# Optimization experiments

Hardware: AMD Instinct MI355X
Metric: run time of the kernel (lower is better)

## Reference

```python
import jax, jax.numpy as jnp
import numpy as np

D_MODEL = 1024
N_HEADS = 16
D_K = D_MODEL // N_HEADS


def setup_inputs() -> dict:
    key = jax.random.key(0)
    ks = jax.random.split(key, 9)
    s = 1.0 / np.sqrt(D_MODEL)
    x = jax.random.normal(ks[0], (2, 2048, D_MODEL), dtype=jnp.float32)
    Wq = jax.random.uniform(ks[1], (D_MODEL, D_MODEL), jnp.float32, -s, s)
    bq = jax.random.uniform(ks[2], (D_MODEL,), jnp.float32, -s, s)
    Wk = jax.random.uniform(ks[3], (D_MODEL, D_MODEL), jnp.float32, -s, s)
    bk = jax.random.uniform(ks[4], (D_MODEL,), jnp.float32, -s, s)
    Wv = jax.random.uniform(ks[5], (D_MODEL, D_MODEL), jnp.float32, -s, s)
    bv = jax.random.uniform(ks[6], (D_MODEL,), jnp.float32, -s, s)
    Wo = jax.random.uniform(ks[7], (D_MODEL, D_MODEL), jnp.float32, -s, s)
    bo = jax.random.uniform(ks[8], (D_MODEL,), jnp.float32, -s, s)
    return {"x": x, "Wq": Wq, "bq": bq, "Wk": Wk, "bk": bk,
            "Wv": Wv, "bv": bv, "Wo": Wo, "bo": bo}


def reference(x, Wq, bq, Wk, bk, Wv, bv, Wo, bo):
    B, S, _ = x.shape
    # torch Linear: y = x @ W.T + b
    def proj(W, b):
        h = x @ W.T + b                       # [B,S,D]
        return h.reshape(B, S, N_HEADS, D_K).transpose(0, 2, 1, 3)  # [B,H,S,dk]
    Q, K, V = proj(Wq, bq), proj(Wk, bk), proj(Wv, bv)
    scale = 1.0 / np.sqrt(D_K).astype(np.float32)
    scores = jnp.einsum('bhqd,bhkd->bhqk', Q, K) * scale  # [B,H,S,S]
    causal = jnp.tril(jnp.ones((S, S), dtype=bool))
    scores = jnp.where(causal, scores, -jnp.inf)
    attn = jax.nn.softmax(scores, axis=-1)
    ctx = jnp.einsum('bhqk,bhkd->bhqd', attn, V)          # [B,H,S,dk]
    ctx = ctx.transpose(0, 2, 1, 3).reshape(B, S, D_MODEL)
    return ctx @ Wo.T + bo
```

## Files before the change

### kernel.cpp

```cpp
#include <hip/hip_runtime.h>
#include <stdint.h>

#define D_MODEL 1024
#define NHEADS  16
#define DKH     64
#define BATCH   2
#define SEQ     2048
#define NTOK    (BATCH*SEQ)

typedef unsigned short u16;
typedef __attribute__((ext_vector_type(8))) short short8;
typedef __attribute__((ext_vector_type(4))) float f32x4;
typedef __attribute__((ext_vector_type(16))) float f32x16;
typedef __attribute__((ext_vector_type(2))) unsigned int u32x2;
typedef __attribute__((address_space(1))) unsigned int as1_u32;
typedef __attribute__((address_space(3))) unsigned int as3_u32;

__device__ __forceinline__ u16 f2bf(float f) {
  unsigned int i = __float_as_uint(f);
  i += 0x7FFF + ((i >> 16) & 1);
  return (u16)(i >> 16);
}
__device__ __forceinline__ f32x4 mfma_bf16(short8 a, short8 b, f32x4 c) {
  return __builtin_amdgcn_mfma_f32_16x16x32_bf16(a, b, c, 0, 0, 0);
}
__device__ __forceinline__ f32x16 mfma32(short8 a, short8 b, f32x16 c) {
  return __builtin_amdgcn_mfma_f32_32x32x16_bf16(a, b, c, 0, 0, 0);
}
__device__ __forceinline__ void gload_lds16(const u16* g, u16* l) {
  __builtin_amdgcn_global_load_lds((as1_u32*)g, (as3_u32*)l, 16, 0, 0);
}
__device__ __forceinline__ short8 ld_frag(const u16* p) {
  short8 v; __builtin_memcpy(&v, __builtin_assume_aligned(p, 16), 16); return v;
}
__device__ __forceinline__ uint32_t pk_bf16_trunc(float hi, float lo) {
  return __builtin_amdgcn_perm(__float_as_uint(hi), __float_as_uint(lo), 0x07060302u);
}

#define QSCALE 0.18033688011112042f
#define M0LOG2 4.32808512266689f

__global__ __launch_bounds__(256)
void convert_kernel(const float* __restrict__ x,  const float* __restrict__ wq,
                    const float* __restrict__ wk, const float* __restrict__ wv,
                    const float* __restrict__ wo,
                    u16* __restrict__ xb,  u16* __restrict__ wqb,
                    u16* __restrict__ wkb, u16* __restrict__ wvb,
                    u16* __restrict__ wob)
{
  const int q = blockIdx.x * 256 + threadIdx.x;
  const float* src; u16* dst; int local;
  if (q < 1048576) { src = x; dst = xb; local = q; }
  else {
    const int t = q - 1048576, r = t >> 18;
    local = t & 262143;
    src = (r == 0) ? wq : (r == 1) ? wk : (r == 2) ? wv : wo;
    dst = (r == 0) ? wqb : (r == 1) ? wkb : (r == 2) ? wvb : wob;
  }
  float f[4];
  __builtin_memcpy(f, src + (size_t)local * 4, 16);
  uint32_t o[2];
  o[0] = ((uint32_t)f2bf(f[1]) << 16) | f2bf(f[0]);
  o[1] = ((uint32_t)f2bf(f[3]) << 16) | f2bf(f[2]);
  __builtin_memcpy(dst + (size_t)local * 4, o, 8);
}

__device__ __forceinline__ void gemm_core_bf16(
    const u16* __restrict__ A, const u16* __restrict__ Bt,
    int m0, int n0, u16* As, u16* Bs, f32x4 (&acc)[4][4])
{
  const int tid  = threadIdx.x;
  const int wave = tid >> 6, lane = tid & 63;
  const int quad = lane >> 4, l15 = lane & 15;
  const int wm = wave & 1, wn = wave >> 1;
  const int srow = lane >> 2;
  const int scol = (lane & 3) << 3;

#pragma unroll
  for (int i = 0; i < 4; i++)
#pragma unroll
    for (int j = 0; j < 4; j++) acc[i][j] = (f32x4){0.f, 0.f, 0.f, 0.f};

  for (int k0 = 0; k0 < D_MODEL; k0 += 32) {
    __syncthreads();
#pragma unroll
    for (int is = 0; is < 2; is++) {
      const int rbase = (is * 4 + wave) * 16;
      gload_lds16(A  + (size_t)(m0 + rbase + srow) * D_MODEL + k0 + scol, As + rbase * 32);
      gload_lds16(Bt + (size_t)(n0 + rbase + srow) * D_MODEL + k0 + scol, Bs + rbase * 32);
    }
    __syncthreads();

    short8 aF[4], bF[4];
#pragma unroll
    for (int i = 0; i < 4; i++)
      aF[i] = ld_frag(As + (wm * 64 + i * 16 + l15) * 32 + quad * 8);
#pragma unroll
    for (int j = 0; j < 4; j++)
      bF[j] = ld_frag(Bs + (wn * 64 + j * 16 + l15) * 32 + quad * 8);
#pragma unroll
    for (int i = 0; i < 4; i++)
#pragma unroll
      for (int j = 0; j < 4; j++)
        acc[i][j] = mfma_bf16(aF[i], bF[j], acc[i][j]);
  }
}

__global__ __launch_bounds__(256)
void qkv_proj_kernel(const u16* __restrict__ xb,
                     const u16* __restrict__ Wqb, const u16* __restrict__ Wkb,
                     const u16* __restrict__ Wvb,
                     const float* __restrict__ bq, const float* __restrict__ bk,
                     const float* __restrict__ bv,
                     u16* __restrict__ qplane, u16* __restrict__ kplane,
                     u16* __restrict__ vplane)
{
  __shared__ __align__(16) u16 SMEM[16384];
  u16* As = SMEM;
  u16* Bs = SMEM + 4096;

  const int m0  = blockIdx.x * 128;
  const int by  = blockIdx.y;
  const int mat = by >> 3;
  const int n0  = (by & 7) * 128;
  const u16* W      = (mat == 0) ? Wqb : (mat == 1) ? Wkb : Wvb;
  const float* bias = (mat == 0) ? bq : (mat == 1) ? bk : bv;

  f32x4 acc[4][4];
  gemm_core_bf16(xb, W, m0, n0, As, Bs, acc);

  const int tid = threadIdx.x, wave = tid >> 6, lane = tid & 63;
  const int quad = lane >> 4, l15 = lane & 15;
  const int wm = wave & 1, wn = wave >> 1;

  if (mat == 0) {
#pragma unroll
    for (int j = 0; j < 4; j++) {
      const int gcol = n0 + wn * 64 + j * 16 + l15;
      const float bias_v = bias[gcol];
      const int h = gcol >> 6, dj = gcol & 63;
#pragma unroll
      for (int i = 0; i < 4; i++) {
#pragma unroll
        for (int r = 0; r < 4; r++) {
          const int grow = m0 + wm * 64 + i * 16 + quad * 4 + r;
          const int b = grow >> 11, s = grow & (SEQ - 1);
          const float v = (acc[i][j][r] + bias_v) * QSCALE;
          qplane[(((size_t)(b * NHEADS + h)) * SEQ + s) * DKH + dj] = f2bf(v);
        }
      }
    }
    return;
  }

  u16* Stg = SMEM;
  __syncthreads();
  const int t4 = (wn * 2 + wm) * 4096;

  if (mat == 1) {
#pragma unroll
    for (int j = 0; j < 4; j++) {
      const int dj = j * 16 + l15;
      const float bias_v = bias[n0 + wn * 64 + dj];
#pragma unroll
      for (int i = 0; i < 4; i++) {
#pragma unroll
        for (int r = 0; r < 4; r++) {
          const int rr = i * 16 + quad * 4 + r;
          Stg[t4 + rr * 64 + (dj ^ ((rr & 7) << 3))] = f2bf(acc[i][j][r] + bias_v);
        }
      }
    }
  } else {
#pragma unroll
    for (int j = 0; j < 4; j++) {
      const int dj = j * 16 + l15;
      const float bias_v = bias[n0 + wn * 64 + dj];
      const int vswz = (dj & 7) << 3;
#pragma unroll
      for (int i = 0; i < 4; i++) {
        const int kkb = i * 16 + quad * 4;
        uint32_t w[2];
        w[0] = ((uint32_t)f2bf(acc[i][j][1] + bias_v) << 16) | f2bf(acc[i][j][0] + bias_v);
        w[1] = ((uint32_t)f2bf(acc[i][j][3] + bias_v) << 16) | f2bf(acc[i][j][2] + bias_v);
        __builtin_memcpy(__builtin_assume_aligned(
            Stg + t4 + dj * 64 + (kkb ^ vswz), 8), w, 8);
      }
    }
  }
  __syncthreads();

  const int tloc = tid >> 6, cl = tid & 63;
  const int hh = tloc >> 1, tt = tloc & 1;
  const int b  = m0 >> 11;
  const int h  = (n0 >> 6) + hh;
  const int kt = ((m0 & (SEQ - 1)) >> 6) + tt;
  u16* gdst = ((mat == 1) ? kplane : vplane)
              + (((size_t)(b * NHEADS + h)) * 32 + kt) * 4096;
  const u16* lsrc = SMEM + tloc * 4096;
#pragma unroll
  for (int ps = 0; ps < 8; ps++) {
    uint32_t tmp[4];
    __builtin_memcpy(tmp, __builtin_assume_aligned(lsrc + ps * 512 + cl * 8, 16), 16);
    __builtin_memcpy(__builtin_assume_aligned(gdst + ps * 512 + cl * 8, 16), tmp, 16);
  }
}


__device__ __forceinline__ void soft_pack(const f32x16& s, const int khBase,
                                          const bool diag, const int qloc,
                                          const int h4, float& l_acc,
                                          short8& fA, short8& fB) {
  float pv[16];
#pragma unroll
  for (int rr = 0; rr < 16; rr++) {
    float v = exp2f(s[rr]);
    if (diag) {
      const int kloc = khBase + (rr & 3) + 8 * (rr >> 2) + h4;
      if (kloc > qloc) v = 0.f;
    }
    pv[rr] = v;
  }
  const float t0 = (pv[0] + pv[1]) + (pv[2] + pv[3]);
  const float t1 = (pv[4] + pv[5]) + (pv[6] + pv[7]);
  const float t2 = (pv[8] + pv[9]) + (pv[10] + pv[11]);
  const float t3 = (pv[12] + pv[13]) + (pv[14] + pv[15]);
  l_acc += (t0 + t1) + (t2 + t3);
  uint32_t w[2][4];
#pragma unroll
  for (int ks = 0; ks < 2; ks++) {
    const uint32_t x0 = pk_bf16_trunc(pv[8 * ks + 1], pv[8 * ks + 0]);
    const uint32_t x1 = pk_bf16_trunc(pv[8 * ks + 3], pv[8 * ks + 2]);
    const uint32_t y0 = pk_bf16_trunc(pv[8 * ks + 5], pv[8 * ks + 4]);
    const uint32_t y1 = pk_bf16_trunc(pv[8 * ks + 7], pv[8 * ks + 6]);
    const u32x2 r0 = __builtin_amdgcn_permlane32_swap(x0, y0, false, false);
    const u32x2 r1 = __builtin_amdgcn_permlane32_swap(x1, y1, false, false);
    w[ks][0] = r0[0]; w[ks][1] = r1[0]; w[ks][2] = r0[1]; w[ks][3] = r1[1];
  }
  __builtin_memcpy(&fA, &w[0][0], 16);
  __builtin_memcpy(&fB, &w[1][0], 16);
}

__device__ __forceinline__ void osum_write(float* OS, const f32x16& o0,
                                           const f32x16& o1, int qb, int l31) {
#pragma unroll
  for (int rr = 0; rr < 16; rr++) {
    const int q = qb + (rr & 3) + 8 * (rr >> 2);
    OS[q * 64 + l31]      = o0[rr];
    OS[q * 64 + 32 + l31] = o1[rr];
  }
}
__device__ __forceinline__ void osum_add(const float* OS, f32x16& o0,
                                         f32x16& o1, int qb, int l31) {
#pragma unroll
  for (int rr = 0; rr < 16; rr++) {
    const int q = qb + (rr & 3) + 8 * (rr >> 2);
    o0[rr] += OS[q * 64 + l31];
    o1[rr] += OS[q * 64 + 32 + l31];
  }
}

__device__ __forceinline__ void stage_tile(const u16* gsrc, u16* ldst,
                                           int w4, int lane8) {
#pragma unroll
  for (int i = 0; i < 2; i++) {
    const int chunk = (w4 * 2 + i) * 512;
    gload_lds16(gsrc + chunk + lane8, ldst + chunk);
  }
}

__global__ __launch_bounds__(512, 4)
void attn_kernel(const u16* __restrict__ Qp, const u16* __restrict__ Kp,
                 const u16* __restrict__ Vp, u16* __restrict__ ctx)
{
  __shared__ __align__(16) u16 Ks[2][2][4096];
  __shared__ __align__(16) u16 Vts[2][2][4096];

  const int xp = blockIdx.x;
  const int bh = blockIdx.y;
  const u16* Q  = Qp + (size_t)bh * SEQ * DKH;
  const u16* Kt = Kp + (size_t)bh * SEQ * DKH;
  const u16* Vt = Vp + (size_t)bh * SEQ * DKH;

  const int tid  = threadIdx.x;
  const int w    = tid >> 6;
  const int lane = tid & 63;
  const int lane8 = lane * 8;
  const int l31  = lane & 31, h = lane >> 5, h8 = h * 8;
  const int g    = w >> 2;
  const int w4   = w & 3;
  const int wq   = (w >> 1) & 1;
  const int kh   = w & 1;
  const int pg   = g * 2 + kh;
  const int b = bh >> 4, hd = bh & 15;
  const int qloc = wq * 32 + l31;
  const int qb   = wq * 32 + h * 4;
  const int xr   = (l31 & 7) << 3;
  const int khB  = kh * 32;

  float* Osum0 = (float*)&Ks[0][0][0];
  float* Osum1 = (float*)&Ks[1][0][0];
  float* Ls    = (float*)&Vts[0][0][0];

#pragma unroll
  for (int p = 0; p < 2; p++) {
    const int qt = p ? xp : 31 - xp;
    const int q0 = qt * 64;
    const int maxR = (qt >> 1) + 1;

    const u16* qrow = Q + (size_t)(q0 + qloc) * DKH + h8;
    const short8 qf0 = ld_frag(qrow + 0);
    const short8 qf1 = ld_frag(qrow + 16);
    const short8 qf2 = ld_frag(qrow + 32);
    const short8 qf3 = ld_frag(qrow + 48);

    __syncthreads();
    const bool act0 = (g <= qt);
    if (act0) {
      stage_tile(Kt + (size_t)g * 4096, &Ks[g][0][0],  w4, lane8);
      stage_tile(Vt + (size_t)g * 4096, &Vts[g][0][0], w4, lane8);
    }
    float l_acc = 0.f;
    f32x16 oacc0, oacc1;
#pragma unroll
    for (int rr = 0; rr < 16; rr++) { oacc0[rr] = 0.f; oacc1[rr] = 0.f; }
    __syncthreads();

    for (int r = 0; r < maxR; r++) {
      const int kt = 2 * r + g;
      const int buf = r & 1;
      const bool act = (kt <= qt);
      if (kt + 2 <= qt) {
        stage_tile(Kt + (size_t)(kt + 2) * 4096, &Ks[g][buf ^ 1][0],  w4, lane8);
        stage_tile(Vt + (size_t)(kt + 2) * 4096, &Vts[g][buf ^ 1][0], w4, lane8);
      }
      if (act) {
        f32x16 s;
#pragma unroll
        for (int rr = 0; rr < 16; rr++) s[rr] = -M0LOG2;
        const u16* kbase = &Ks[g][buf][0] + (size_t)(khB + l31) * 64;
        s = mfma32(ld_frag(kbase + ((0  + h8) ^ xr)), qf0, s);
        s = mfma32(ld_frag(kbase + ((16 + h8) ^ xr)), qf1, s);
        s = mfma32(ld_frag(kbase + ((32 + h8) ^ xr)), qf2, s);
        s = mfma32(ld_frag(kbase + ((48 + h8) ^ xr)), qf3, s);
        short8 pa0, pa1;
        soft_pack(s, khB, kt == qt, qloc, h * 4, l_acc, pa0, pa1);
        const u16* v0 = &Vts[g][buf][0] + (size_t)l31 * 64;
        const u16* v1 = &Vts[g][buf][0] + (size_t)(32 + l31) * 64;
        oacc0 = mfma32(pa0, ld_frag(v0 + ((khB + 0  + h8) ^ xr)), oacc0);
        oacc1 = mfma32(pa0, ld_frag(v1 + ((khB + 0  + h8) ^ xr)), oacc1);
        oacc0 = mfma32(pa1, ld_frag(v0 + ((khB + 16 + h8) ^ xr)), oacc0);
        oacc1 = mfma32(pa1, ld_frag(v1 + ((khB + 16 + h8) ^ xr)), oacc1);
      }
      __syncthreads();
    }

    l_acc += __shfl_xor(l_acc, 32);
    if (lane < 32) Ls[pg * 64 + wq * 32 + l31] = l_acc;
    if (pg == 1) osum_write(Osum0, oacc0, oacc1, qb, l31);
    if (pg == 3) osum_write(Osum1, oacc0, oacc1, qb, l31);
    __syncthreads();
    if (pg == 0) osum_add(Osum0, oacc0, oacc1, qb, l31);
    if (pg == 2) osum_add(Osum1, oacc0, oacc1, qb, l31);
    if (w == 1) {
      const float sum = Ls[lane] + Ls[64 + lane] + Ls[128 + lane] + Ls[192 + lane];
      Ls[lane] = 1.f / sum;
    }
    __syncthreads();
    if (pg == 2) osum_write(Osum0, oacc0, oacc1, qb, l31);
    __syncthreads();
    if (pg == 0) {
#pragma unroll
      for (int rr = 0; rr < 16; rr++) {
        const int q = qb + (rr & 3) + 8 * (rr >> 2);
        const float linv = Ls[q];
        u16* dst = ctx + ((size_t)(b * SEQ + q0 + q)) * D_MODEL + hd * DKH;
        dst[l31]      = f2bf((oacc0[rr] + Osum0[q * 64 + l31]) * linv);
        dst[32 + l31] = f2bf((oacc1[rr] + Osum0[q * 64 + 32 + l31]) * linv);
      }
    }
  }
}

__global__ __launch_bounds__(256)
void oproj_kernel(const u16* __restrict__ ctx, const u16* __restrict__ Wob,
                  const float* __restrict__ bo, float* __restrict__ out)
{
  __shared__ __align__(16) u16 As[128 * 32];
  __shared__ __align__(16) u16 Bs[128 * 32];
  const int m0 = blockIdx.x * 128, n0 = blockIdx.y * 128;

  f32x4 acc[4][4];
  gemm_core_bf16(ctx, Wob, m0, n0, As, Bs, acc);

  const int tid = threadIdx.x, wave = tid >> 6, lane = tid & 63;
  const int quad = lane >> 4, l15 = lane & 15;
  const int wm = wave & 1, wn = wave >> 1;
#pragma unroll
  for (int j = 0; j < 4; j++) {
    const int gcol = n0 + wn * 64 + j * 16 + l15;
    const float bias_v = bo[gcol];
#pragma unroll
    for (int i = 0; i < 4; i++) {
#pragma unroll
      for (int r = 0; r < 4; r++) {
        const int grow = m0 + wm * 64 + i * 16 + quad * 4 + r;
        out[(size_t)grow * D_MODEL + gcol] = acc[i][j][r] + bias_v;
      }
    }
  }
}

extern "C" void kernel_launch(void* const* d_in, const int* in_sizes, int n_in,
                              void* d_out, int out_size, void* d_ws, size_t ws_size,
                              hipStream_t stream) {
  const float* x  = (const float*)d_in[0];
  const float* Wq = (const float*)d_in[1];
  const float* bq = (const float*)d_in[2];
  const float* Wk = (const float*)d_in[3];
  const float* bk = (const float*)d_in[4];
  const float* Wv = (const float*)d_in[5];
  const float* bv = (const float*)d_in[6];
  const float* Wo = (const float*)d_in[7];
  const float* bo = (const float*)d_in[8];
  u16*   ws   = (u16*)d_ws;
  u16*   o16  = (u16*)d_out;
  float* out  = (float*)d_out;

  const size_t plane = (size_t)NTOK * D_MODEL;
  u16* Kp  = ws;
  u16* Vp  = ws + plane;
  u16* xb  = ws + 2 * plane;
  u16* ctx = ws + 2 * plane;
  u16* Wob = ws + 3 * plane;
  u16* Qp  = o16;
  u16* Wqb = o16 + 4 * 1048576;
  u16* Wkb = o16 + 5 * 1048576;
  u16* Wvb = o16 + 6 * 1048576;

  convert_kernel<<<dim3(8192), dim3(256), 0, stream>>>(x, Wq, Wk, Wv, Wo,
                                                       xb, Wqb, Wkb, Wvb, Wob);
  qkv_proj_kernel<<<dim3(32, 24), dim3(256), 0, stream>>>(xb, Wqb, Wkb, Wvb,
                                                          bq, bk, bv, Qp, Kp, Vp);
  attn_kernel<<<dim3(16, 32), dim3(512), 0, stream>>>(Qp, Kp, Vp, ctx);
  oproj_kernel<<<dim3(32, 8), dim3(256), 0, stream>>>(ctx, Wob, bo, out);
}
```

Measured before the change: 199.4 us.

## Fuse Q/K/V projections into one kernel sharing the x tile

Replaces the per-matrix QKV projection grid (32x24 blocks of 256 threads) with a fused kernel (32x8 blocks of 512 threads). Each block loads one x tile and the matching Q, K and V weight tiles, and accumulates all three outputs, so every A tile is loaded once instead of three times. The K-loop is now double-buffered with async global-to-LDS loads. The trade-off is fewer blocks (256), larger LDS use (64KB) and more accumulator registers per thread, which may reduce occupancy and parallelism on the GPU.

```diff
diff --git a/kernel.cpp b/kernel.cpp
--- a/kernel.cpp
+++ b/kernel.cpp
@@ -106,103 +106,156 @@
   }
 }
 
-__global__ __launch_bounds__(256)
-void qkv_proj_kernel(const u16* __restrict__ xb,
-                     const u16* __restrict__ Wqb, const u16* __restrict__ Wkb,
-                     const u16* __restrict__ Wvb,
-                     const float* __restrict__ bq, const float* __restrict__ bk,
-                     const float* __restrict__ bv,
-                     u16* __restrict__ qplane, u16* __restrict__ kplane,
-                     u16* __restrict__ vplane)
+__global__ __launch_bounds__(512)
+void qkv_fused_kernel(const u16* __restrict__ xb,
+                      const u16* __restrict__ Wqb, const u16* __restrict__ Wkb,
+                      const u16* __restrict__ Wvb,
+                      const float* __restrict__ bq, const float* __restrict__ bk,
+                      const float* __restrict__ bv,
+                      u16* __restrict__ qplane, u16* __restrict__ kplane,
+                      u16* __restrict__ vplane)
 {
-  __shared__ __align__(16) u16 SMEM[16384];
-  u16* As = SMEM;
-  u16* Bs = SMEM + 4096;
-
-  const int m0  = blockIdx.x * 128;
-  const int by  = blockIdx.y;
-  const int mat = by >> 3;
-  const int n0  = (by & 7) * 128;
-  const u16* W      = (mat == 0) ? Wqb : (mat == 1) ? Wkb : Wvb;
-  const float* bias = (mat == 0) ? bq : (mat == 1) ? bk : bv;
-
-  f32x4 acc[4][4];
-  gemm_core_bf16(xb, W, m0, n0, As, Bs, acc);
-
-  const int tid = threadIdx.x, wave = tid >> 6, lane = tid & 63;
+  __shared__ __align__(16) u16 SM[32768];
+  u16* As = SM;
+  u16* Bq = SM + 8192;
+  u16* Bk = SM + 16384;
+  u16* Bv = SM + 24576;
+
+  const int m0 = blockIdx.x * 128;
+  const int n0 = blockIdx.y * 128;
+
+  const int tid  = threadIdx.x;
+  const int wave = tid >> 6, lane = tid & 63;
   const int quad = lane >> 4, l15 = lane & 15;
-  const int wm = wave & 1, wn = wave >> 1;
-
-  if (mat == 0) {
-#pragma unroll
-    for (int j = 0; j < 4; j++) {
-      const int gcol = n0 + wn * 64 + j * 16 + l15;
-      const float bias_v = bias[gcol];
-      const int h = gcol >> 6, dj = gcol & 63;
+  const int wm = wave & 1;
+  const int wn = wave >> 1;
+  const int srow = lane >> 2;
+  const int scol = (lane & 3) << 3;
+  const int wrow = wave * 16 + srow;
+  const int ldso = wave * 512;
+
+  const u16* srcA = xb  + (size_t)(m0 + wrow) * D_MODEL + scol;
+  const u16* srcQ = Wqb + (size_t)(n0 + wrow) * D_MODEL + scol;
+  const u16* srcK = Wkb + (size_t)(n0 + wrow) * D_MODEL + scol;
+  const u16* srcV = Wvb + (size_t)(n0 + wrow) * D_MODEL + scol;
+
+  f32x4 accQ[4][2], accK[4][2], accV[4][2];
+#pragma unroll
+  for (int i = 0; i < 4; i++)
+#pragma unroll
+    for (int j = 0; j < 2; j++) {
+      accQ[i][j] = (f32x4){0.f, 0.f, 0.f, 0.f};
+      accK[i][j] = (f32x4){0.f, 0.f, 0.f, 0.f};
+      accV[i][j] = (f32x4){0.f, 0.f, 0.f, 0.f};
+    }
+
+  gload_lds16(srcA, As + ldso);
+  gload_lds16(srcQ, Bq + ldso);
+  gload_lds16(srcK, Bk + ldso);
+  gload_lds16(srcV, Bv + ldso);
+  __syncthreads();
+
+  for (int k0 = 0; k0 < D_MODEL; k0 += 32) {
+    const int buf = (k0 >> 5) & 1;
+    if (k0 + 32 < D_MODEL) {
+      const int nb = (buf ^ 1) * 4096 + ldso;
+      gload_lds16(srcA + k0 + 32, As + nb);
+      gload_lds16(srcQ + k0 + 32, Bq + nb);
+      gload_lds16(srcK + k0 + 32, Bk + nb);
+      gload_lds16(srcV + k0 + 32, Bv + nb);
+    }
+    const int bo = buf * 4096;
+    short8 aF[4];
+#pragma unroll
+    for (int i = 0; i < 4; i++)
+      aF[i] = ld_frag(As + bo + (wm * 64 + i * 16 + l15) * 32 + quad * 8);
+    {
+      const short8 b0 = ld_frag(Bq + bo + (wn * 32 + l15) * 32 + quad * 8);
+      const short8 b1 = ld_frag(Bq + bo + (wn * 32 + 16 + l15) * 32 + quad * 8);
 #pragma unroll
       for (int i = 0; i < 4; i++) {
-#pragma unroll
-        for (int r = 0; r < 4; r++) {
-          const int grow = m0 + wm * 64 + i * 16 + quad * 4 + r;
-          const int b = grow >> 11, s = grow & (SEQ - 1);
-          const float v = (acc[i][j][r] + bias_v) * QSCALE;
-          qplane[(((size_t)(b * NHEADS + h)) * SEQ + s) * DKH + dj] = f2bf(v);
-        }
-      }
-    }
-    return;
-  }
-
-  u16* Stg = SMEM;
+        accQ[i][0] = mfma_bf16(aF[i], b0, accQ[i][0]);
+        accQ[i][1] = mfma_bf16(aF[i], b1, accQ[i][1]);
+      }
+    }
+    {
+      const short8 b0 = ld_frag(Bk + bo + (wn * 32 + l15) * 32 + quad * 8);
+      const short8 b1 = ld_frag(Bk + bo + (wn * 32 + 16 + l15) * 32 + quad * 8);
+#pragma unroll
+      for (int i = 0; i < 4; i++) {
+        accK[i][0] = mfma_bf16(aF[i], b0, accK[i][0]);
+        accK[i][1] = mfma_bf16(aF[i], b1, accK[i][1]);
+      }
+    }
+    {
+      const short8 b0 = ld_frag(Bv + bo + (wn * 32 + l15) * 32 + quad * 8);
+      const short8 b1 = ld_frag(Bv + bo + (wn * 32 + 16 + l15) * 32 + quad * 8);
+#pragma unroll
+      for (int i = 0; i < 4; i++) {
+        accV[i][0] = mfma_bf16(aF[i], b0, accV[i][0]);
+        accV[i][1] = mfma_bf16(aF[i], b1, accV[i][1]);
+      }
+    }
+    __syncthreads();
+  }
+
+  u16* KStg = SM;
+  u16* VStg = SM + 16384;
+  const int t4 = ((wn >> 1) * 2 + wm) * 4096;
+
+#pragma unroll
+  for (int j = 0; j < 2; j++) {
+    const int gcol = n0 + wn * 32 + j * 16 + l15;
+    const int dj = gcol & 63;
+    const float bkv = bk[gcol];
+    const float bvv = bv[gcol];
+    const int vswz = (dj & 7) << 3;
+#pragma unroll
+    for (int i = 0; i < 4; i++) {
+#pragma unroll
+      for (int r = 0; r < 4; r++) {
+        const int rr = i * 16 + quad * 4 + r;
+        KStg[t4 + rr * 64 + (dj ^ ((rr & 7) << 3))] = f2bf(accK[i][j][r] + bkv);
+      }
+      const int kkb = i * 16 + quad * 4;
+      uint32_t w2[2];
+      w2[0] = ((uint32_t)f2bf(accV[i][j][1] + bvv) << 16) | f2bf(accV[i][j][0] + bvv);
+      w2[1] = ((uint32_t)f2bf(accV[i][j][3] + bvv) << 16) | f2bf(accV[i][j][2] + bvv);
+      __builtin_memcpy(__builtin_assume_aligned(
+          VStg + t4 + dj * 64 + (kkb ^ vswz), 8), w2, 8);
+    }
+  }
   __syncthreads();
-  const int t4 = (wn * 2 + wm) * 4096;
-
-  if (mat == 1) {
-#pragma unroll
-    for (int j = 0; j < 4; j++) {
-      const int dj = j * 16 + l15;
-      const float bias_v = bias[n0 + wn * 64 + dj];
-#pragma unroll
-      for (int i = 0; i < 4; i++) {
-#pragma unroll
-        for (int r = 0; r < 4; r++) {
-          const int rr = i * 16 + quad * 4 + r;
-          Stg[t4 + rr * 64 + (dj ^ ((rr & 7) << 3))] = f2bf(acc[i][j][r] + bias_v);
-        }
-      }
-    }
-  } else {
-#pragma unroll
-    for (int j = 0; j < 4; j++) {
-      const int dj = j * 16 + l15;
-      const float bias_v = bias[n0 + wn * 64 + dj];
-      const int vswz = (dj & 7) << 3;
-#pragma unroll
-      for (int i = 0; i < 4; i++) {
-        const int kkb = i * 16 + quad * 4;
-        uint32_t w[2];
-        w[0] = ((uint32_t)f2bf(acc[i][j][1] + bias_v) << 16) | f2bf(acc[i][j][0] + bias_v);
-        w[1] = ((uint32_t)f2bf(acc[i][j][3] + bias_v) << 16) | f2bf(acc[i][j][2] + bias_v);
-        __builtin_memcpy(__builtin_assume_aligned(
-            Stg + t4 + dj * 64 + (kkb ^ vswz), 8), w, 8);
-      }
-    }
-  }
-  __syncthreads();
-
-  const int tloc = tid >> 6, cl = tid & 63;
-  const int hh = tloc >> 1, tt = tloc & 1;
+
+#pragma unroll
+  for (int j = 0; j < 2; j++) {
+    const int gcol = n0 + wn * 32 + j * 16 + l15;
+    const float bqv = bq[gcol];
+    const int h = gcol >> 6, dj = gcol & 63;
+#pragma unroll
+    for (int i = 0; i < 4; i++) {
+#pragma unroll
+      for (int r = 0; r < 4; r++) {
+        const int grow = m0 + wm * 64 + i * 16 + quad * 4 + r;
+        const int b = grow >> 11, s = grow & (SEQ - 1);
+        qplane[(((size_t)(b * NHEADS + h)) * SEQ + s) * DKH + dj] =
+            f2bf((accQ[i][j][r] + bqv) * QSCALE);
+      }
+    }
+  }
+
+  const int hh = (wave & 3) >> 1, tt = wave & 1;
   const int b  = m0 >> 11;
   const int h  = (n0 >> 6) + hh;
   const int kt = ((m0 & (SEQ - 1)) >> 6) + tt;
-  u16* gdst = ((mat == 1) ? kplane : vplane)
+  u16* gdst = ((wave < 4) ? kplane : vplane)
               + (((size_t)(b * NHEADS + h)) * 32 + kt) * 4096;
-  const u16* lsrc = SMEM + tloc * 4096;
+  const u16* lsrc = SM + wave * 4096;
 #pragma unroll
   for (int ps = 0; ps < 8; ps++) {
     uint32_t tmp[4];
-    __builtin_memcpy(tmp, __builtin_assume_aligned(lsrc + ps * 512 + cl * 8, 16), 16);
-    __builtin_memcpy(__builtin_assume_aligned(gdst + ps * 512 + cl * 8, 16), tmp, 16);
+    __builtin_memcpy(tmp, __builtin_assume_aligned(lsrc + ps * 512 + lane * 8, 16), 16);
+    __builtin_memcpy(__builtin_assume_aligned(gdst + ps * 512 + lane * 8, 16), tmp, 16);
   }
 }
 
@@ -440,7 +493,7 @@
 
   convert_kernel<<<dim3(8192), dim3(256), 0, stream>>>(x, Wq, Wk, Wv, Wo,
                                                        xb, Wqb, Wkb, Wvb, Wob);
-  qkv_proj_kernel<<<dim3(32, 24), dim3(256), 0, stream>>>(xb, Wqb, Wkb, Wvb,
+  qkv_fused_kernel<<<dim3(32, 8), dim3(512), 0, stream>>>(xb, Wqb, Wkb, Wvb,
                                                           bq, bk, bv, Qp, Kp, Vp);
   attn_kernel<<<dim3(16, 32), dim3(512), 0, stream>>>(Qp, Kp, Vp, ctx);
   oproj_kernel<<<dim3(32, 8), dim3(256), 0, stream>>>(ctx, Wob, bo, out);
```

New measurement: 196.4 us. About the same (-1.5%).
